# Performance work log

Measured on AMD Instinct MI355X. Metric: run time of the kernel, lower is better.

Reference implementation:

```python
import jax, jax.numpy as jnp
import numpy as np

N_NODES = 100000
N_EDGES = 1600000
NEG_SLOPE = 0.2


def _gat_conv(x, src, dst, W, att_src, att_dst, bias, heads, out_ch):
    """PyG-style GATConv (eval mode, self-loops already in src/dst)."""
    n = x.shape[0]
    h = (x @ W).reshape(n, heads, out_ch)            # [N,H,C]
    a_src = jnp.sum(h * att_src, axis=-1)            # [N,H]
    a_dst = jnp.sum(h * att_dst, axis=-1)            # [N,H]
    e = jax.nn.leaky_relu(a_src[src] + a_dst[dst], NEG_SLOPE)  # [E,H]
    # segment softmax over destination nodes
    m = jax.ops.segment_max(e, dst, num_segments=n)  # [N,H]
    ex = jnp.exp(e - m[dst])                         # [E,H]
    denom = jax.ops.segment_sum(ex, dst, num_segments=n)  # [N,H]
    alpha = ex / (denom[dst] + 1e-16)                # [E,H]
    # weighted scatter-aggregate of source features
    out = jax.ops.segment_sum(alpha[:, :, None] * h[src], dst, num_segments=n)  # [N,H,C]
    return out.reshape(n, heads * out_ch) + bias


def setup_inputs() -> dict:
    key = jax.random.key(0)
    ks = jax.random.split(key, 10)
    nfeat, nhid, nclass, heads = 128, 16, 40, 8
    return {
        "x": jax.random.normal(ks[0], (N_NODES, nfeat), jnp.float32),
        "edge_index": jax.random.randint(ks[1], (2, N_EDGES), 0, N_NODES, jnp.int64),
        "W1": jax.random.normal(ks[2], (nfeat, heads * nhid), jnp.float32) * 0.1,
        "att_src1": jax.random.normal(ks[3], (1, heads, nhid), jnp.float32) * 0.1,
        "att_dst1": jax.random.normal(ks[4], (1, heads, nhid), jnp.float32) * 0.1,
        "b1": jax.random.normal(ks[5], (heads * nhid,), jnp.float32) * 0.1,
        "W2": jax.random.normal(ks[6], (heads * nhid, nclass), jnp.float32) * 0.1,
        "att_src2": jax.random.normal(ks[7], (1, 1, nclass), jnp.float32) * 0.1,
        "att_dst2": jax.random.normal(ks[8], (1, 1, nclass), jnp.float32) * 0.1,
        "b2": jax.random.normal(ks[9], (nclass,), jnp.float32) * 0.1,
    }


def reference(x, edge_index, W1, att_src1, att_dst1, b1, W2, att_src2, att_dst2, b2):
    n = x.shape[0]
    # add self loops (PyG GATConv default)
    loops = jnp.arange(n, dtype=edge_index.dtype)
    src = jnp.concatenate([edge_index[0], loops])
    dst = jnp.concatenate([edge_index[1], loops])
    # dropout p=0.6 is a no-op in eval mode
    h = _gat_conv(x, src, dst, W1, att_src1, att_dst1, b1, heads=8, out_ch=16)
    h = jax.nn.elu(h)
    out = _gat_conv(h, src, dst, W2, att_src2, att_dst2, b2, heads=1, out_ch=40)
    return jax.nn.log_softmax(out, axis=1)
```

## Files before the change

kernel.cpp:

```cpp
#include <hip/hip_runtime.h>
#include <math.h>


#define NPB   32
#define G     8
#define RCAP  192
#define BSTRIDE (G*RCAP)
#define EPT   8

__device__ __forceinline__ float wave_max(float v){
  #pragma unroll
  for (int m = 1; m < 64; m <<= 1) v = fmaxf(v, __shfl_xor(v, m));
  return v;
}
__device__ __forceinline__ float wave_sum(float v){
  #pragma unroll
  for (int m = 1; m < 64; m <<= 1) v += __shfl_xor(v, m);
  return v;
}
__device__ __forceinline__ int lane_bcast_i(int v, int l){
  return __builtin_amdgcn_readlane(v, l);
}
__device__ __forceinline__ float lane_bcast_f(float v, int l){
  return __uint_as_float((unsigned)__builtin_amdgcn_readlane(__float_as_int(v), l));
}

__device__ __forceinline__ unsigned short f2bf(float f){
  unsigned int u = __float_as_uint(f);
  u += 0x7FFFu + ((u >> 16) & 1u);
  return (unsigned short)(u >> 16);
}
__device__ __forceinline__ float bf2f(unsigned short b){
  return __uint_as_float(((unsigned int)b) << 16);
}
__device__ __forceinline__ float2 bfpair(unsigned int u){
  float2 r;
  r.x = __uint_as_float(u << 16);
  r.y = __uint_as_float(u & 0xFFFF0000u);
  return r;
}


__global__ void zero_bcnt_kernel(int* __restrict__ p, int nr){
  int i = blockIdx.x * 256 + threadIdx.x;
  if (i < nr) p[i] = 0;
}

__global__ void binA_kernel(const int* __restrict__ src, const int* __restrict__ dst,
                            int* __restrict__ bcnt, unsigned int* __restrict__ bdata,
                            int E, int tot){
  int base = blockIdx.x * (256 * EPT) + threadIdx.x;
  int rep = blockIdx.x & (G - 1);
  unsigned pk[EPT]; int rr[EPT]; int pos[EPT];
  #pragma unroll
  for (int k = 0; k < EPT; k++){
    int i = base + k * 256;
    rr[k] = -1; pk[k] = 0u;
    if (i < tot){
      int s, d;
      if (i < E){ s = src[i]; d = dst[i]; } else { s = i - E; d = s; }
      rr[k] = (d >> 5) * G + rep;
      pk[k] = (unsigned)s | ((unsigned)(d & 31) << 17);
    }
  }
  #pragma unroll
  for (int k = 0; k < EPT; k++)
    pos[k] = (rr[k] >= 0) ? atomicAdd(&bcnt[rr[k]], 1) : 0;
  #pragma unroll
  for (int k = 0; k < EPT; k++)
    if (rr[k] >= 0 && pos[k] < RCAP)
      bdata[(size_t)rr[k] * RCAP + pos[k]] = pk[k];
}

__global__ __launch_bounds__(256)
void binB_kernel(const int* __restrict__ bcnt, const unsigned int* __restrict__ bdata,
                 int* __restrict__ offs, int* __restrict__ cntg,
                 int* __restrict__ col, int n){
  __shared__ int hist[NPB];
  __shared__ int sc[NPB];
  __shared__ int curp[NPB];
  int tid = threadIdx.x;
  int b = blockIdx.x;
  int base_node = b * NPB;

  if (tid < NPB) hist[tid] = 0;
  __syncthreads();
  #pragma unroll
  for (int g = 0; g < G; g++){
    int rc = bcnt[b * G + g]; if (rc > RCAP) rc = RCAP;
    size_t rb = (size_t)(b * G + g) * RCAP;
    for (int j = tid; j < rc; j += 256)
      atomicAdd(&hist[bdata[rb + j] >> 17], 1);
  }
  __syncthreads();
  if (tid < NPB) sc[tid] = hist[tid];
  __syncthreads();
  #pragma unroll
  for (int d1 = 1; d1 < NPB; d1 <<= 1){
    int v = 0;
    if (tid < NPB && tid >= d1) v = sc[tid - d1];
    __syncthreads();
    if (tid < NPB) sc[tid] += v;
    __syncthreads();
  }
  if (tid < NPB){
    int ex = tid ? sc[tid - 1] : 0;
    int node = base_node + tid;
    if (node < n){
      offs[node] = b * BSTRIDE + ex;
      cntg[node] = hist[tid];
    }
    curp[tid] = ex;
  }
  __syncthreads();
  #pragma unroll
  for (int g = 0; g < G; g++){
    int rc = bcnt[b * G + g]; if (rc > RCAP) rc = RCAP;
    size_t rb = (size_t)(b * G + g) * RCAP;
    for (int j = tid; j < rc; j += 256){
      unsigned int u = bdata[rb + j];
      int r = atomicAdd(&curp[u >> 17], 1);
      col[b * BSTRIDE + r] = (int)(u & 0x1FFFFu);
    }
  }
}

__global__ __launch_bounds__(256)
void gemm1_kernel(const float* __restrict__ X, const float* __restrict__ W,
                  unsigned short* __restrict__ Hb, int n){
  __shared__ float xs[16][132];
  __shared__ float ws[16][128];
  int tid = threadIdx.x;
  int rg = tid >> 4, cg = tid & 15;
  int r0 = rg * 8, c0 = cg * 4;
  int row0 = blockIdx.x * 128;
  float acc[8][8];
  #pragma unroll
  for (int i = 0; i < 8; i++)
    #pragma unroll
    for (int j = 0; j < 8; j++) acc[i][j] = 0.f;

  for (int k0 = 0; k0 < 128; k0 += 16){
    #pragma unroll
    for (int l = 0; l < 2; l++){
      int f4 = tid + l * 256;
      int kk = f4 >> 5, cq = f4 & 31;
      float4 w = *(const float4*)(W + (size_t)(k0 + kk) * 128 + cq * 4);
      *(float4*)&ws[kk][cq * 4] = w;
    }
    #pragma unroll
    for (int l = 0; l < 2; l++){
      int f4 = tid + l * 256;
      int row = f4 >> 2, kq = f4 & 3;
      float4 v = make_float4(0.f, 0.f, 0.f, 0.f);
      if (row0 + row < n)
        v = *(const float4*)(X + (size_t)(row0 + row) * 128 + k0 + kq * 4);
      xs[kq*4+0][row] = v.x; xs[kq*4+1][row] = v.y;
      xs[kq*4+2][row] = v.z; xs[kq*4+3][row] = v.w;
    }
    __syncthreads();
    #pragma unroll
    for (int k = 0; k < 16; k++){
      float4 xa = *(const float4*)&xs[k][r0];
      float4 xb = *(const float4*)&xs[k][r0 + 4];
      float4 wa = *(const float4*)&ws[k][c0];
      float4 wb = *(const float4*)&ws[k][c0 + 64];
      float xr[8] = {xa.x,xa.y,xa.z,xa.w,xb.x,xb.y,xb.z,xb.w};
      float wr[8] = {wa.x,wa.y,wa.z,wa.w,wb.x,wb.y,wb.z,wb.w};
      #pragma unroll
      for (int i = 0; i < 8; i++)
        #pragma unroll
        for (int j = 0; j < 8; j++)
          acc[i][j] = fmaf(xr[i], wr[j], acc[i][j]);
    }
    __syncthreads();
  }
  #pragma unroll
  for (int i = 0; i < 8; i++){
    int r = row0 + r0 + i;
    if (r < n){
      ushort4 a4, b4;
      a4.x = f2bf(acc[i][0]); a4.y = f2bf(acc[i][1]);
      a4.z = f2bf(acc[i][2]); a4.w = f2bf(acc[i][3]);
      b4.x = f2bf(acc[i][4]); b4.y = f2bf(acc[i][5]);
      b4.z = f2bf(acc[i][6]); b4.w = f2bf(acc[i][7]);
      *(ushort4*)(Hb + (size_t)r * 128 + c0)      = a4;
      *(ushort4*)(Hb + (size_t)r * 128 + c0 + 64) = b4;
    }
  }
}

__global__ __launch_bounds__(256)
void att1_kernel(const unsigned short* __restrict__ Hb, const float* __restrict__ As,
                 const float* __restrict__ Ad, float* __restrict__ asrc,
                 float* __restrict__ adst, int n){
  __shared__ float sa[128], sd[128];
  int tid = threadIdx.x;
  if (tid < 128){ sa[tid] = As[tid]; sd[tid] = Ad[tid]; }
  __syncthreads();
  int t = blockIdx.x * 256 + tid;
  if (t >= n * 8) return;
  int node = t >> 3, h = t & 7;
  const uint4* hp = (const uint4*)(Hb + (size_t)node * 128 + h * 16);
  uint4 u0 = hp[0], u1 = hp[1];
  unsigned int w[8] = {u0.x,u0.y,u0.z,u0.w,u1.x,u1.y,u1.z,u1.w};
  float s = 0.f, d = 0.f;
  #pragma unroll
  for (int q = 0; q < 8; q++){
    float2 p = bfpair(w[q]);
    s = fmaf(p.x, sa[h*16 + 2*q],     s);
    s = fmaf(p.y, sa[h*16 + 2*q + 1], s);
    d = fmaf(p.x, sd[h*16 + 2*q],     d);
    d = fmaf(p.y, sd[h*16 + 2*q + 1], d);
  }
  asrc[t] = s; adst[t] = d;
}

__global__ __launch_bounds__(256)
void agg1_kernel(const unsigned short* __restrict__ Hb, const int* __restrict__ offs,
                 const int* __restrict__ cnt, const int* __restrict__ col,
                 const float* __restrict__ asrc, const float* __restrict__ adst,
                 const float* __restrict__ bias, float* __restrict__ G1, int n){
  int lane = threadIdx.x & 63;
  int wid  = threadIdx.x >> 6;
  int node = blockIdx.x * 4 + wid;
  if (node >= n) return;
  int beg = offs[node], deg = cnt[node];

  int hA = lane & 7, iA = lane >> 3;
  int hB = lane >> 3;
  float adA = adst[(unsigned)node * 8u + hA];
  const unsigned int* Hu = (const unsigned int*)Hb;

  float2 acc = make_float2(0.f, 0.f);
  float m_run = -INFINITY;
  float denomA = 0.f;

  for (int c0 = 0; c0 < deg; c0 += 64){
    int cdeg = min(64, deg - c0);
    int sv[8]; float xv[8];
    float cm = -INFINITY;
    #pragma unroll
    for (int k = 0; k < 8; k++){
      int i = iA + k * 8;
      sv[k] = 0; xv[k] = -INFINITY;
      if (i < cdeg){
        int s = col[beg + c0 + i];
        sv[k] = s;
        float e = asrc[(unsigned)s * 8u + hA] + adA;
        e = e > 0.f ? e : 0.2f * e;
        xv[k] = e;
        cm = fmaxf(cm, e);
      }
    }
    cm = fmaxf(cm, __shfl_xor(cm, 8));
    cm = fmaxf(cm, __shfl_xor(cm, 16));
    cm = fmaxf(cm, __shfl_xor(cm, 32));
    float m_new = fmaxf(m_run, cm);
    float scaleA = __expf(m_run - m_new);
    denomA *= scaleA;
    #pragma unroll
    for (int k = 0; k < 8; k++){
      int i = iA + k * 8;
      if (i < cdeg){
        float ex = __expf(xv[k] - m_new);
        xv[k] = ex;
        denomA += ex;
      } else xv[k] = 0.f;
    }
    m_run = m_new;
    float scaleB = __shfl(scaleA, hB);
    acc.x *= scaleB; acc.y *= scaleB;
    #pragma unroll
    for (int k = 0; k < 8; k++){
      if (k * 8 >= cdeg) break;
      int sk[8]; float ek[8]; unsigned fu[8];
      #pragma unroll
      for (int j = 0; j < 8; j++){
        sk[j] = lane_bcast_i(sv[k], j * 8);
        ek[j] = __shfl(xv[k], j * 8 + hB);
      }
      #pragma unroll
      for (int j = 0; j < 8; j++)
        fu[j] = Hu[(unsigned)sk[j] * 64u + lane];
      #pragma unroll
      for (int j = 0; j < 8; j++){
        float2 f = bfpair(fu[j]);
        acc.x = fmaf(ek[j], f.x, acc.x);
        acc.y = fmaf(ek[j], f.y, acc.y);
      }
    }
  }
  denomA += __shfl_xor(denomA, 8);
  denomA += __shfl_xor(denomA, 16);
  denomA += __shfl_xor(denomA, 32);
  float denomB = __shfl(denomA, hB) + 1e-16f;
  float2 bv = ((const float2*)bias)[lane];
  float ox = acc.x / denomB + bv.x;
  float oy = acc.y / denomB + bv.y;
  ox = ox > 0.f ? ox : __expf(ox) - 1.f;
  oy = oy > 0.f ? oy : __expf(oy) - 1.f;
  ((float2*)G1)[(size_t)node * 64 + lane] = make_float2(ox, oy);
}

__global__ __launch_bounds__(256)
void gemm2_kernel(const float* __restrict__ X, const float* __restrict__ W,
                  unsigned short* __restrict__ Hb, int n){
  __shared__ float xs[16][132];
  __shared__ float ws[16][48];
  int tid = threadIdx.x;
  int rg = tid >> 3, cg = tid & 7;
  int r0 = rg * 4, c0 = cg * 6;
  int row0 = blockIdx.x * 128;
  float acc[4][6];
  #pragma unroll
  for (int i = 0; i < 4; i++)
    #pragma unroll
    for (int j = 0; j < 6; j++) acc[i][j] = 0.f;

  for (int k0 = 0; k0 < 128; k0 += 16){
    #pragma unroll
    for (int l = 0; l < 3; l++){
      int idx = tid + l * 256;
      int kk = idx / 48, c = idx % 48;
      ws[kk][c] = (c < 40) ? W[(size_t)(k0 + kk) * 40 + c] : 0.f;
    }
    #pragma unroll
    for (int l = 0; l < 2; l++){
      int f4 = tid + l * 256;
      int row = f4 >> 2, kq = f4 & 3;
      float4 v = make_float4(0.f, 0.f, 0.f, 0.f);
      if (row0 + row < n)
        v = *(const float4*)(X + (size_t)(row0 + row) * 128 + k0 + kq * 4);
      xs[kq*4+0][row] = v.x; xs[kq*4+1][row] = v.y;
      xs[kq*4+2][row] = v.z; xs[kq*4+3][row] = v.w;
    }
    __syncthreads();
    #pragma unroll
    for (int k = 0; k < 16; k++){
      float4 xa = *(const float4*)&xs[k][r0];
      float xr[4] = {xa.x, xa.y, xa.z, xa.w};
      float wr[6];
      #pragma unroll
      for (int j = 0; j < 6; j++) wr[j] = ws[k][c0 + j];
      #pragma unroll
      for (int i = 0; i < 4; i++)
        #pragma unroll
        for (int j = 0; j < 6; j++)
          acc[i][j] = fmaf(xr[i], wr[j], acc[i][j]);
    }
    __syncthreads();
  }
  #pragma unroll
  for (int i = 0; i < 4; i++){
    int r = row0 + r0 + i;
    if (r < n){
      #pragma unroll
      for (int j = 0; j < 6; j++){
        int c = c0 + j;
        if (c < 40) Hb[(size_t)r * 40 + c] = f2bf(acc[i][j]);
      }
    }
  }
}

__global__ __launch_bounds__(256)
void att2_kernel(const unsigned short* __restrict__ Hb, const float* __restrict__ As,
                 const float* __restrict__ Ad, float* __restrict__ asrc,
                 float* __restrict__ adst, int n){
  int lane = threadIdx.x & 63;
  int node = blockIdx.x * 4 + (threadIdx.x >> 6);
  if (node >= n) return;
  float v = 0.f, a = 0.f, d = 0.f;
  if (lane < 40){
    v = bf2f(Hb[(size_t)node * 40 + lane]);
    a = As[lane];
    d = Ad[lane];
  }
  float s1 = wave_sum(v * a);
  float s2 = wave_sum(v * d);
  if (lane == 0){ asrc[node] = s1; adst[node] = s2; }
}

__global__ __launch_bounds__(256)
void agg2_kernel(const unsigned short* __restrict__ Hb, const int* __restrict__ offs,
                 const int* __restrict__ cnt, const int* __restrict__ col,
                 const float* __restrict__ asrc, const float* __restrict__ adst,
                 const float* __restrict__ bias, float* __restrict__ out, int n){
  int lane = threadIdx.x & 63;
  int wid  = threadIdx.x >> 6;
  int node = blockIdx.x * 4 + wid;
  if (node >= n) return;
  int beg = offs[node], deg = cnt[node];
  float ad = adst[node];
  unsigned choff = (lane < 40) ? (unsigned)lane : 0u;

  float acc = 0.f;
  float m_run = -INFINITY;
  float denom = 0.f;

  for (int c0 = 0; c0 < deg; c0 += 64){
    int cdeg = min(64, deg - c0);
    int s = 0; float ev = -INFINITY;
    if (lane < cdeg){
      s = col[beg + c0 + lane];
      float e = asrc[s] + ad;
      ev = e > 0.f ? e : 0.2f * e;
    }
    float cm = wave_max(ev);
    float m_new = fmaxf(m_run, cm);
    float scale = __expf(m_run - m_new);
    float ex = (lane < cdeg) ? __expf(ev - m_new) : 0.f;
    denom = denom * scale + wave_sum(ex);
    acc *= scale;
    m_run = m_new;
    #pragma unroll
    for (int kb = 0; kb < 8; kb++){
      if (kb * 8 >= cdeg) break;
      int sk[8]; float ek[8]; unsigned short fv[8];
      #pragma unroll
      for (int j = 0; j < 8; j++){
        int k = kb * 8 + j;
        sk[j] = lane_bcast_i(s, k);
        ek[j] = lane_bcast_f(ex, k);
      }
      #pragma unroll
      for (int j = 0; j < 8; j++)
        fv[j] = Hb[(unsigned)sk[j] * 40u + choff];
      #pragma unroll
      for (int j = 0; j < 8; j++)
        acc = fmaf(ek[j], bf2f(fv[j]), acc);
    }
  }
  float val = 0.f;
  if (lane < 40) val = acc / (denom + 1e-16f) + bias[lane];

  float mx = wave_max(lane < 40 ? val : -INFINITY);
  float ssum = wave_sum(lane < 40 ? __expf(val - mx) : 0.f);
  float ls = logf(ssum);
  if (lane < 40) out[(size_t)node * 40 + lane] = val - mx - ls;
}

extern "C" void kernel_launch(void* const* d_in, const int* in_sizes, int n_in,
                              void* d_out, int out_size, void* d_ws, size_t ws_size,
                              hipStream_t stream){
  const float* x   = (const float*)d_in[0];
  const int*   ei  = (const int*)d_in[1];
  const float* W1  = (const float*)d_in[2];
  const float* as1 = (const float*)d_in[3];
  const float* ad1 = (const float*)d_in[4];
  const float* b1  = (const float*)d_in[5];
  const float* W2  = (const float*)d_in[6];
  const float* as2 = (const float*)d_in[7];
  const float* ad2 = (const float*)d_in[8];
  const float* b2  = (const float*)d_in[9];
  float* out = (float*)d_out;

  int n = in_sizes[0] / 128;
  int E = in_sizes[1] / 2;
  const int* src = ei;
  const int* dst = ei + E;
  int tot = E + n;
  int nb = (n + NPB - 1) / NPB;
  int nr = nb * G;

  char* w = (char*)d_ws;
  size_t off = 0;
  auto alloc = [&](size_t bytes){
    size_t r = off; off += (bytes + 255) & ~(size_t)255; return r;
  };
  int* bcnt = (int*)(w + alloc((size_t)nr * 4));
  unsigned int* bdata = (unsigned int*)(w + alloc((size_t)nr * RCAP * 4));
  int* offs = (int*)(w + alloc((size_t)n * 4));
  int* cnt  = (int*)(w + alloc((size_t)n * 4));
  int* col  = (int*)(w + alloc((size_t)nb * BSTRIDE * 4));
  unsigned short* h1b = (unsigned short*)(w + alloc((size_t)n * 128 * 2));
  float* g1   = (float*)(w + alloc((size_t)n * 128 * 4));
  float* s1   = (float*)(w + alloc((size_t)n * 8 * 4));
  float* t1   = (float*)(w + alloc((size_t)n * 8 * 4));
  unsigned short* h2b = h1b;
  float* s2 = s1;
  float* t2 = t1;
  (void)ws_size; (void)n_in; (void)out_size;

  zero_bcnt_kernel<<<(nr + 255) / 256, 256, 0, stream>>>(bcnt, nr);
  int nba = (tot + 256 * EPT - 1) / (256 * EPT);
  binA_kernel<<<nba, 256, 0, stream>>>(src, dst, bcnt, bdata, E, tot);
  binB_kernel<<<nb, 256, 0, stream>>>(bcnt, bdata, offs, cnt, col, n);

  gemm1_kernel<<<(n + 127) / 128, 256, 0, stream>>>(x, W1, h1b, n);
  att1_kernel<<<(n * 8 + 255) / 256, 256, 0, stream>>>(h1b, as1, ad1, s1, t1, n);
  agg1_kernel<<<(n + 3) / 4, 256, 0, stream>>>(h1b, offs, cnt, col, s1, t1, b1, g1, n);

  gemm2_kernel<<<(n + 127) / 128, 256, 0, stream>>>(g1, W2, h2b, n);
  att2_kernel<<<(n + 3) / 4, 256, 0, stream>>>(h2b, as2, ad2, s2, t2, n);
  agg2_kernel<<<(n + 3) / 4, 256, 0, stream>>>(h2b, offs, cnt, col, s2, t2, b2, out, n);
}
```

Baseline: 465.5 us.

## Fuse edge binning with GEMM1 and attention-logit epilogues into GEMM kernels

```diff
diff --git a/kernel.cpp b/kernel.cpp
--- a/kernel.cpp
+++ b/kernel.cpp
@@ -40,100 +40,50 @@
   return r;
 }
 
-
 __global__ void zero_bcnt_kernel(int* __restrict__ p, int nr){
   int i = blockIdx.x * 256 + threadIdx.x;
   if (i < nr) p[i] = 0;
 }
 
-__global__ void binA_kernel(const int* __restrict__ src, const int* __restrict__ dst,
-                            int* __restrict__ bcnt, unsigned int* __restrict__ bdata,
-                            int E, int tot){
-  int base = blockIdx.x * (256 * EPT) + threadIdx.x;
-  int rep = blockIdx.x & (G - 1);
-  unsigned pk[EPT]; int rr[EPT]; int pos[EPT];
-  #pragma unroll
-  for (int k = 0; k < EPT; k++){
-    int i = base + k * 256;
-    rr[k] = -1; pk[k] = 0u;
-    if (i < tot){
-      int s, d;
-      if (i < E){ s = src[i]; d = dst[i]; } else { s = i - E; d = s; }
-      rr[k] = (d >> 5) * G + rep;
-      pk[k] = (unsigned)s | ((unsigned)(d & 31) << 17);
-    }
-  }
-  #pragma unroll
-  for (int k = 0; k < EPT; k++)
-    pos[k] = (rr[k] >= 0) ? atomicAdd(&bcnt[rr[k]], 1) : 0;
-  #pragma unroll
-  for (int k = 0; k < EPT; k++)
-    if (rr[k] >= 0 && pos[k] < RCAP)
-      bdata[(size_t)rr[k] * RCAP + pos[k]] = pk[k];
-}
-
 __global__ __launch_bounds__(256)
-void binB_kernel(const int* __restrict__ bcnt, const unsigned int* __restrict__ bdata,
-                 int* __restrict__ offs, int* __restrict__ cntg,
-                 int* __restrict__ col, int n){
-  __shared__ int hist[NPB];
-  __shared__ int sc[NPB];
-  __shared__ int curp[NPB];
-  int tid = threadIdx.x;
-  int b = blockIdx.x;
-  int base_node = b * NPB;
-
-  if (tid < NPB) hist[tid] = 0;
-  __syncthreads();
-  #pragma unroll
-  for (int g = 0; g < G; g++){
-    int rc = bcnt[b * G + g]; if (rc > RCAP) rc = RCAP;
-    size_t rb = (size_t)(b * G + g) * RCAP;
-    for (int j = tid; j < rc; j += 256)
-      atomicAdd(&hist[bdata[rb + j] >> 17], 1);
-  }
-  __syncthreads();
-  if (tid < NPB) sc[tid] = hist[tid];
-  __syncthreads();
-  #pragma unroll
-  for (int d1 = 1; d1 < NPB; d1 <<= 1){
-    int v = 0;
-    if (tid < NPB && tid >= d1) v = sc[tid - d1];
-    __syncthreads();
-    if (tid < NPB) sc[tid] += v;
-    __syncthreads();
-  }
-  if (tid < NPB){
-    int ex = tid ? sc[tid - 1] : 0;
-    int node = base_node + tid;
-    if (node < n){
-      offs[node] = b * BSTRIDE + ex;
-      cntg[node] = hist[tid];
-    }
-    curp[tid] = ex;
-  }
-  __syncthreads();
-  #pragma unroll
-  for (int g = 0; g < G; g++){
-    int rc = bcnt[b * G + g]; if (rc > RCAP) rc = RCAP;
-    size_t rb = (size_t)(b * G + g) * RCAP;
-    for (int j = tid; j < rc; j += 256){
-      unsigned int u = bdata[rb + j];
-      int r = atomicAdd(&curp[u >> 17], 1);
-      col[b * BSTRIDE + r] = (int)(u & 0x1FFFFu);
-    }
-  }
-}
-
-__global__ __launch_bounds__(256)
-void gemm1_kernel(const float* __restrict__ X, const float* __restrict__ W,
-                  unsigned short* __restrict__ Hb, int n){
+void fused1_kernel(const int* __restrict__ src, const int* __restrict__ dst,
+                   int* __restrict__ bcnt, unsigned int* __restrict__ bdata,
+                   int E, int tot, int nba, int nb,
+                   const float* __restrict__ X, const float* __restrict__ W,
+                   unsigned short* __restrict__ Hb,
+                   const float* __restrict__ As, const float* __restrict__ Ad,
+                   float* __restrict__ asrc, float* __restrict__ adst, int n){
   __shared__ float xs[16][132];
   __shared__ float ws[16][128];
+  if ((int)blockIdx.x < nba){
+    int base = blockIdx.x * (256 * EPT) + threadIdx.x;
+    int rep = blockIdx.x & (G - 1);
+    unsigned pk[EPT]; int rr[EPT]; int pos[EPT];
+    #pragma unroll
+    for (int k = 0; k < EPT; k++){
+      int i = base + k * 256;
+      rr[k] = -1; pk[k] = 0u;
+      if (i < tot){
+        int s, d;
+        if (i < E){ s = src[i]; d = dst[i]; } else { s = i - E; d = s; }
+        rr[k] = rep * nb + (d >> 5);
+        pk[k] = (unsigned)s | ((unsigned)(d & 31) << 17);
+      }
+    }
+    #pragma unroll
+    for (int k = 0; k < EPT; k++)
+      pos[k] = (rr[k] >= 0) ? atomicAdd(&bcnt[rr[k]], 1) : 0;
+    #pragma unroll
+    for (int k = 0; k < EPT; k++)
+      if (rr[k] >= 0 && pos[k] < RCAP)
+        bdata[(size_t)rr[k] * RCAP + pos[k]] = pk[k];
+    return;
+  }
+  int bid = blockIdx.x - nba;
   int tid = threadIdx.x;
   int rg = tid >> 4, cg = tid & 15;
   int r0 = rg * 8, c0 = cg * 4;
-  int row0 = blockIdx.x * 128;
+  int row0 = bid * 128;
   float acc[8][8];
   #pragma unroll
   for (int i = 0; i < 8; i++)
@@ -188,32 +138,80 @@
       *(ushort4*)(Hb + (size_t)r * 128 + c0 + 64) = b4;
     }
   }
+  float4 a0 = *(const float4*)(As + cg * 4);
+  float4 a1 = *(const float4*)(As + 64 + cg * 4);
+  float4 d0 = *(const float4*)(Ad + cg * 4);
+  float4 d1 = *(const float4*)(Ad + 64 + cg * 4);
+  int hL = cg >> 2, hH = 4 + (cg >> 2);
+  #pragma unroll
+  for (int i = 0; i < 8; i++){
+    int r = row0 + r0 + i;
+    float sL = acc[i][0]*a0.x + acc[i][1]*a0.y + acc[i][2]*a0.z + acc[i][3]*a0.w;
+    float sH = acc[i][4]*a1.x + acc[i][5]*a1.y + acc[i][6]*a1.z + acc[i][7]*a1.w;
+    float tL = acc[i][0]*d0.x + acc[i][1]*d0.y + acc[i][2]*d0.z + acc[i][3]*d0.w;
+    float tH = acc[i][4]*d1.x + acc[i][5]*d1.y + acc[i][6]*d1.z + acc[i][7]*d1.w;
+    sL += __shfl_xor(sL, 1); sL += __shfl_xor(sL, 2);
+    sH += __shfl_xor(sH, 1); sH += __shfl_xor(sH, 2);
+    tL += __shfl_xor(tL, 1); tL += __shfl_xor(tL, 2);
+    tH += __shfl_xor(tH, 1); tH += __shfl_xor(tH, 2);
+    if ((cg & 3) == 0 && r < n){
+      asrc[r * 8 + hL] = sL; asrc[r * 8 + hH] = sH;
+      adst[r * 8 + hL] = tL; adst[r * 8 + hH] = tH;
+    }
+  }
 }
 
 __global__ __launch_bounds__(256)
-void att1_kernel(const unsigned short* __restrict__ Hb, const float* __restrict__ As,
-                 const float* __restrict__ Ad, float* __restrict__ asrc,
-                 float* __restrict__ adst, int n){
-  __shared__ float sa[128], sd[128];
+void binB_kernel(const int* __restrict__ bcnt, const unsigned int* __restrict__ bdata,
+                 int* __restrict__ offs, int* __restrict__ cntg,
+                 int* __restrict__ col, int n, int nb){
+  __shared__ int hist[NPB];
+  __shared__ int sc[NPB];
+  __shared__ int curp[NPB];
   int tid = threadIdx.x;
-  if (tid < 128){ sa[tid] = As[tid]; sd[tid] = Ad[tid]; }
+  int b = blockIdx.x;
+  int base_node = b * NPB;
+
+  if (tid < NPB) hist[tid] = 0;
   __syncthreads();
-  int t = blockIdx.x * 256 + tid;
-  if (t >= n * 8) return;
-  int node = t >> 3, h = t & 7;
-  const uint4* hp = (const uint4*)(Hb + (size_t)node * 128 + h * 16);
-  uint4 u0 = hp[0], u1 = hp[1];
-  unsigned int w[8] = {u0.x,u0.y,u0.z,u0.w,u1.x,u1.y,u1.z,u1.w};
-  float s = 0.f, d = 0.f;
-  #pragma unroll
-  for (int q = 0; q < 8; q++){
-    float2 p = bfpair(w[q]);
-    s = fmaf(p.x, sa[h*16 + 2*q],     s);
-    s = fmaf(p.y, sa[h*16 + 2*q + 1], s);
-    d = fmaf(p.x, sd[h*16 + 2*q],     d);
-    d = fmaf(p.y, sd[h*16 + 2*q + 1], d);
-  }
-  asrc[t] = s; adst[t] = d;
+  #pragma unroll
+  for (int g = 0; g < G; g++){
+    int rc = bcnt[g * nb + b]; if (rc > RCAP) rc = RCAP;
+    size_t rb = (size_t)(g * nb + b) * RCAP;
+    for (int j = tid; j < rc; j += 256)
+      atomicAdd(&hist[bdata[rb + j] >> 17], 1);
+  }
+  __syncthreads();
+  if (tid < NPB) sc[tid] = hist[tid];
+  __syncthreads();
+  #pragma unroll
+  for (int d1 = 1; d1 < NPB; d1 <<= 1){
+    int v = 0;
+    if (tid < NPB && tid >= d1) v = sc[tid - d1];
+    __syncthreads();
+    if (tid < NPB) sc[tid] += v;
+    __syncthreads();
+  }
+  if (tid < NPB){
+    int ex = tid ? sc[tid - 1] : 0;
+    int node = base_node + tid;
+    if (node < n){
+      offs[node] = b * BSTRIDE + ex;
+      cntg[node] = hist[tid];
+    }
+    curp[tid] = ex;
+  }
+  __syncthreads();
+  #pragma unroll
+  for (int g = 0; g < G; g++){
+    int rc = bcnt[g * nb + b]; if (rc > RCAP) rc = RCAP;
+    size_t rb = (size_t)(g * nb + b) * RCAP;
+    for (int j = tid; j < rc; j += 256){
+      unsigned int u = bdata[rb + j];
+      int r = atomicAdd(&curp[u >> 17], 1);
+      col[b * BSTRIDE + r] = (int)(u & 0x1FFFFu);
+    }
+  }
 }
 
 __global__ __launch_bounds__(256)
@@ -305,7 +303,9 @@
 
 __global__ __launch_bounds__(256)
 void gemm2_kernel(const float* __restrict__ X, const float* __restrict__ W,
-                  unsigned short* __restrict__ Hb, int n){
+                  unsigned short* __restrict__ Hb,
+                  const float* __restrict__ As2, const float* __restrict__ Ad2,
+                  float* __restrict__ asrc2, float* __restrict__ adst2, int n){
   __shared__ float xs[16][132];
   __shared__ float ws[16][48];
   int tid = threadIdx.x;
@@ -362,24 +362,26 @@
       }
     }
   }
-}
-
-__global__ __launch_bounds__(256)
-void att2_kernel(const unsigned short* __restrict__ Hb, const float* __restrict__ As,
-                 const float* __restrict__ Ad, float* __restrict__ asrc,
-                 float* __restrict__ adst, int n){
-  int lane = threadIdx.x & 63;
-  int node = blockIdx.x * 4 + (threadIdx.x >> 6);
-  if (node >= n) return;
-  float v = 0.f, a = 0.f, d = 0.f;
-  if (lane < 40){
-    v = bf2f(Hb[(size_t)node * 40 + lane]);
-    a = As[lane];
-    d = Ad[lane];
-  }
-  float s1 = wave_sum(v * a);
-  float s2 = wave_sum(v * d);
-  if (lane == 0){ asrc[node] = s1; adst[node] = s2; }
+  float av[6], dv[6];
+  #pragma unroll
+  for (int j = 0; j < 6; j++){
+    int c = c0 + j;
+    av[j] = (c < 40) ? As2[c] : 0.f;
+    dv[j] = (c < 40) ? Ad2[c] : 0.f;
+  }
+  #pragma unroll
+  for (int i = 0; i < 4; i++){
+    int r = row0 + r0 + i;
+    float s = 0.f, t = 0.f;
+    #pragma unroll
+    for (int j = 0; j < 6; j++){
+      s = fmaf(acc[i][j], av[j], s);
+      t = fmaf(acc[i][j], dv[j], t);
+    }
+    s += __shfl_xor(s, 1); s += __shfl_xor(s, 2); s += __shfl_xor(s, 4);
+    t += __shfl_xor(t, 1); t += __shfl_xor(t, 2); t += __shfl_xor(t, 4);
+    if (cg == 0 && r < n){ asrc2[r] = s; adst2[r] = t; }
+  }
 }
 
 __global__ __launch_bounds__(256)
@@ -485,14 +487,14 @@
 
   zero_bcnt_kernel<<<(nr + 255) / 256, 256, 0, stream>>>(bcnt, nr);
   int nba = (tot + 256 * EPT - 1) / (256 * EPT);
-  binA_kernel<<<nba, 256, 0, stream>>>(src, dst, bcnt, bdata, E, tot);
-  binB_kernel<<<nb, 256, 0, stream>>>(bcnt, bdata, offs, cnt, col, n);
-
-  gemm1_kernel<<<(n + 127) / 128, 256, 0, stream>>>(x, W1, h1b, n);
-  att1_kernel<<<(n * 8 + 255) / 256, 256, 0, stream>>>(h1b, as1, ad1, s1, t1, n);
+  int ngm = (n + 127) / 128;
+  fused1_kernel<<<nba + ngm, 256, 0, stream>>>(src, dst, bcnt, bdata, E, tot,
+                                               nba, nb, x, W1, h1b,
+                                               as1, ad1, s1, t1, n);
+  binB_kernel<<<nb, 256, 0, stream>>>(bcnt, bdata, offs, cnt, col, n, nb);
+
   agg1_kernel<<<(n + 3) / 4, 256, 0, stream>>>(h1b, offs, cnt, col, s1, t1, b1, g1, n);
 
-  gemm2_kernel<<<(n + 127) / 128, 256, 0, stream>>>(g1, W2, h2b, n);
-  att2_kernel<<<(n + 3) / 4, 256, 0, stream>>>(h2b, as2, ad2, s2, t2, n);
+  gemm2_kernel<<<ngm, 256, 0, stream>>>(g1, W2, h2b, as2, ad2, s2, t2, n);
   agg2_kernel<<<(n + 3) / 4, 256, 0, stream>>>(h2b, offs, cnt, col, s2, t2, b2, out, n);
 }
```

Result: faster. 437.8 us (-6.0%).
